# Optimization experiments

Measured on AMD Instinct MI355X. Metric: run time of the kernel, lower is better.

## Reference

```python
import jax, jax.numpy as jnp
import numpy as np

DIM = 384
PATCH = [(4, 4), (8, 8), (16, 16)]  # (width, height) per channel chunk
B, H, W = 4, 192, 192


def setup_inputs() -> dict:
    key = jax.random.key(0)
    ks = jax.random.split(key, 6)
    c = DIM
    return {
        "rgb": jax.random.normal(ks[0], (B, c, H, W), jnp.float32),
        "fre": jax.random.normal(ks[1], (B, c, H, W), jnp.float32),
        # shared BatchNorm2d (eval-mode affine) applied to both rgb and fre
        "norm_gamma": jnp.ones((c,), jnp.float32),
        "norm_beta": jnp.zeros((c,), jnp.float32),
        "norm_mean": jnp.zeros((c,), jnp.float32),
        "norm_var": jnp.ones((c,), jnp.float32),
        # qv: Conv2d(c, 2c, 1); k: Conv2d(c, c, 1)
        "qv_w": jax.random.normal(ks[2], (2 * c, c), jnp.float32) * 0.02,
        "qv_b": jnp.zeros((2 * c,), jnp.float32),
        "k_w": jax.random.normal(ks[3], (c, c), jnp.float32) * 0.02,
        "k_b": jnp.zeros((c,), jnp.float32),
        # out_conv: Conv2d(c, c, 3, padding=1, bias=False) + BN + LeakyReLU(0.2)
        "oc_w": jax.random.normal(ks[4], (c, c, 3, 3), jnp.float32) * 0.02,
        "oc_gamma": jnp.ones((c,), jnp.float32),
        "oc_beta": jnp.zeros((c,), jnp.float32),
        "oc_mean": jnp.zeros((c,), jnp.float32),
        "oc_var": jnp.ones((c,), jnp.float32),
    }


def _bn(x, g, b, m, v, eps=1e-5):
    scale = g * jax.lax.rsqrt(v + eps)
    return x * scale[None, :, None, None] + (b - m * scale)[None, :, None, None]


def _conv1x1(x, w, b):
    return jnp.einsum('bchw,oc->bohw', x, w) + b[None, :, None, None]


def _win_attn(q, k, v, ww, wh, scale):
    # q,k,v: [b, d, h, w]; window of size (wh x ww)
    b, d, h, w = q.shape
    gh, gw = h // wh, w // ww

    def to_win(t):  # -> [b, gh*gw, wh*ww, d]
        t = t.reshape(b, d, gh, wh, gw, ww).transpose(0, 2, 4, 3, 5, 1)
        return t.reshape(b, gh * gw, wh * ww, d)

    qw, kw, vw = to_win(q), to_win(k), to_win(v)
    attn = jax.nn.softmax((qw * scale) @ kw.swapaxes(-2, -1), axis=-1)
    o = (attn @ vw).reshape(b, gh, gw, wh, ww, d)
    return o.transpose(0, 5, 1, 3, 2, 4).reshape(b, d, h, w)


def reference(rgb, fre, norm_gamma, norm_beta, norm_mean, norm_var,
              qv_w, qv_b, k_w, k_b, oc_w, oc_gamma, oc_beta, oc_mean, oc_var):
    b, c, h, w = rgb.shape
    n = len(PATCH)
    d_k = c // n
    scale = d_k ** (-0.5)

    qv = _conv1x1(_bn(rgb, norm_gamma, norm_beta, norm_mean, norm_var), qv_w, qv_b)
    q, v = qv[:, :c], qv[:, c:]  # reshape(b,2,c,h,w) ordering -> first c = q, next c = v
    k = _conv1x1(_bn(fre, norm_gamma, norm_beta, norm_mean, norm_var), k_w, k_b)

    outs = []
    for i, (ww, wh) in enumerate(PATCH):
        sl = slice(i * d_k, (i + 1) * d_k)
        o = _win_attn(q[:, sl], k[:, sl], v[:, sl], ww, wh, scale) + rgb[:, sl]
        outs.append(o)
    x = jnp.concatenate(outs, axis=1)

    x = jax.lax.conv_general_dilated(x, oc_w, (1, 1), 'SAME',
                                     dimension_numbers=('NCHW', 'OIHW', 'NCHW'))
    x = _bn(x, oc_gamma, oc_beta, oc_mean, oc_var)
    return jnp.where(x >= 0, x, 0.2 * x)  # LeakyReLU(0.2)
```

## Files before the change

### kernel.cpp

```cpp
#include <hip/hip_runtime.h>
#include <stdint.h>

typedef __attribute__((ext_vector_type(8))) short short8;
typedef __attribute__((ext_vector_type(8))) unsigned short ushort8;
typedef __attribute__((ext_vector_type(4))) float f32x4;

#define MFMA(a,b,c) __builtin_amdgcn_mfma_f32_16x16x32_bf16((a),(b),(c),0,0,0)

__device__ __forceinline__ unsigned short f2bf(float f) {
  union { float f; unsigned u; } v; v.f = f;
  unsigned r = v.u + 0x7fffu + ((v.u >> 16) & 1u);
  return (unsigned short)(r >> 16);
}
__device__ __forceinline__ float bf2f(unsigned short s) {
  union { unsigned u; float f; } v; v.u = ((unsigned)s) << 16;
  return v.f;
}

__device__ __forceinline__ void g2l16(const unsigned short* g, unsigned short* l) {
  __builtin_amdgcn_global_load_lds(
      (const __attribute__((address_space(1))) unsigned int*)(g),
      (__attribute__((address_space(3))) unsigned int*)(l), 16, 0, 0);
}

__device__ __forceinline__ int vswz(int c, int key) {
  return key ^ ((((c >> 3) ^ c) & 7) << 3);
}

__global__ void nhwc_kernel(const float* __restrict__ src, unsigned short* __restrict__ dst) {
  __shared__ unsigned short T[64][72];
  int p0 = blockIdx.x * 64, c0 = blockIdx.y * 64, bb = blockIdx.z;
  const float* S = src + (size_t)bb * 384 * 36864;
  unsigned short* D = dst + (size_t)bb * 36864 * 384;
  int t = threadIdx.x;
  int pl = (t & 15) * 4;
  int r0 = t >> 4;
#pragma unroll
  for (int k = 0; k < 4; ++k) {
    int c = r0 + 16 * k;
    float4 v = *(const float4*)&S[(size_t)(c0 + c) * 36864 + p0 + pl];
    T[pl + 0][c] = f2bf(v.x); T[pl + 1][c] = f2bf(v.y);
    T[pl + 2][c] = f2bf(v.z); T[pl + 3][c] = f2bf(v.w);
  }
  __syncthreads();
  int row = t >> 2, ch = (t & 3) * 16;
  ushort8 a = *(const ushort8*)&T[row][ch];
  ushort8 b = *(const ushort8*)&T[row][ch + 8];
  uint4* d = (uint4*)&D[(size_t)(p0 + row) * 384 + c0 + ch];
  d[0] = *(uint4*)&a; d[1] = *(uint4*)&b;
}

__global__ void fold_qvk_kernel(const float* __restrict__ qv_w, const float* __restrict__ qv_b,
                                const float* __restrict__ k_w, const float* __restrict__ k_b,
                                const float* __restrict__ g, const float* __restrict__ be,
                                const float* __restrict__ mu, const float* __restrict__ var,
                                unsigned short* __restrict__ Wq, float* __restrict__ bq,
                                unsigned short* __restrict__ Wk, float* __restrict__ bk) {
  int o = blockIdx.x;
  int t = threadIdx.x;
  bool isq = o < 768;
  int oo = isq ? o : o - 768;
  const float* wrow = isq ? qv_w + (size_t)oo * 384 : k_w + (size_t)oo * 384;
  float mul = (isq && oo < 384) ? 0.08838834764831845f : 1.0f;
  float acc = 0.f;
  for (int c = t; c < 384; c += 128) {
    float sc = g[c] * rsqrtf(var[c] + 1e-5f);
    float sh = be[c] - mu[c] * sc;
    float w = wrow[c];
    acc += w * sh;
    unsigned short wb = f2bf(w * sc * mul);
    if (isq) Wq[(size_t)oo * 384 + c] = wb; else Wk[(size_t)oo * 384 + c] = wb;
  }
#pragma unroll
  for (int m = 1; m < 64; m <<= 1) acc += __shfl_xor(acc, m);
  __shared__ float part[2];
  if ((t & 63) == 0) part[t >> 6] = acc;
  __syncthreads();
  if (t == 0) {
    float b0 = isq ? qv_b[oo] : k_b[oo];
    float bias = (b0 + part[0] + part[1]) * mul;
    if (isq) bq[oo] = bias; else bk[oo] = bias;
  }
}

__global__ void fold_oc_kernel(const float* __restrict__ oc_w,
                               const float* __restrict__ g, const float* __restrict__ be,
                               const float* __restrict__ mu, const float* __restrict__ var,
                               unsigned short* __restrict__ Wc, float* __restrict__ s_oc,
                               float* __restrict__ t_oc) {
  int idx = blockIdx.x * 256 + threadIdx.x;
  if (idx < 384) {
    float sc = g[idx] * rsqrtf(var[idx] + 1e-5f);
    s_oc[idx] = sc;
    t_oc[idx] = be[idx] - mu[idx] * sc;
  }
  if (idx < 384 * 3456) {
    int o = idx / 3456, r = idx % 3456;
    int kq = r / 384, c = r % 384;
    Wc[idx] = f2bf(oc_w[((size_t)o * 384 + c) * 9 + kq]);
  }
}

__launch_bounds__(512)
__global__ void gemm1n_kernel(const unsigned short* __restrict__ XN, const unsigned short* __restrict__ W,
                              const float* __restrict__ bias, unsigned short* __restrict__ Out,
                              int OW, int OT) {
  int nwg = gridDim.x;
  int bid = blockIdx.x;
  int bi = (bid & 7) * (nwg >> 3) + (bid >> 3);
  int ot = bi % OT;
  int pt = (bi / OT) % 144;
  int bb = bi / (OT * 144);
  int obase = ot * 128, pbase = pt * 256;
  __shared__ unsigned short Ws2[2][128 * 32];
  __shared__ unsigned short Xs2[2][256 * 32];
  int tid = threadIdx.x;
  int wv = tid >> 6, lane = tid & 63;
  int l15 = lane & 15, lg = lane >> 4;
  int wc = wv & 1, wr = wv >> 1;
  f32x4 acc[4][4];
#pragma unroll
  for (int i = 0; i < 4; ++i)
#pragma unroll
    for (int j = 0; j < 4; ++j) acc[i][j] = 0.f;
  int rl = lane >> 2;
  int csw = (((lane & 3) ^ ((lane >> 3) & 3)) << 3);
  const unsigned short* Ap = W + (size_t)(obase + 16 * wv + rl) * 384 + csw;
  const unsigned short* XbN = XN + (size_t)bb * 36864 * 384;
  const unsigned short* Bp0 = XbN + (size_t)(pbase + 32 * wv + rl) * 384 + csw;
  const unsigned short* Bp1 = Bp0 + (size_t)16 * 384;
  int colsw = ((lg ^ ((l15 >> 1) & 3)) << 3);
  unsigned short* WsW = &Ws2[0][(16 * wv) * 32];
  unsigned short* XsW0 = &Xs2[0][(32 * wv) * 32];
  unsigned short* XsW1 = &Xs2[0][(32 * wv + 16) * 32];
  const int WBUF = 128 * 32, XBUF = 256 * 32;
  g2l16(Ap, WsW); g2l16(Bp0, XsW0); g2l16(Bp1, XsW1);
  Ap += 32; Bp0 += 32; Bp1 += 32;
  for (int t = 0; t < 12; ++t) {
    int cur = t & 1, nxt = cur ^ 1;
    if (t < 11) {
      g2l16(Ap, WsW + nxt * WBUF);
      g2l16(Bp0, XsW0 + nxt * XBUF);
      g2l16(Bp1, XsW1 + nxt * XBUF);
      Ap += 32; Bp0 += 32; Bp1 += 32;
      asm volatile("s_waitcnt vmcnt(3)" ::: "memory");
    } else {
      asm volatile("s_waitcnt vmcnt(0)" ::: "memory");
    }
    __builtin_amdgcn_s_barrier();
    __builtin_amdgcn_sched_barrier(0);
    const unsigned short* Wt = &Ws2[cur][0];
    const unsigned short* Xt = &Xs2[cur][0];
    short8 af[4], bf[4];
#pragma unroll
    for (int f = 0; f < 4; ++f) af[f] = *(const short8*)&Xt[(wr * 64 + f * 16 + l15) * 32 + colsw];
#pragma unroll
    for (int f = 0; f < 4; ++f) bf[f] = *(const short8*)&Wt[(wc * 64 + f * 16 + l15) * 32 + colsw];
#pragma unroll
    for (int fm = 0; fm < 4; ++fm)
#pragma unroll
      for (int fn = 0; fn < 4; ++fn)
        acc[fm][fn] = MFMA(af[fm], bf[fn], acc[fm][fn]);
    __builtin_amdgcn_s_barrier();
    __builtin_amdgcn_sched_barrier(0);
  }
  unsigned short* Ob = Out + (size_t)bb * 36864 * OW;
#pragma unroll
  for (int fn = 0; fn < 4; ++fn) {
    int o = obase + wc * 64 + fn * 16 + l15;
    float bsv = bias[o];
#pragma unroll
    for (int fm = 0; fm < 4; ++fm) {
#pragma unroll
      for (int r = 0; r < 4; ++r) {
        int p = pbase + wr * 64 + fm * 16 + lg * 4 + r;
        Ob[(size_t)p * OW + o] = f2bf(acc[fm][fn][r] + bsv);
      }
    }
  }
}

__launch_bounds__(256)
__global__ void gemm1_kernel(const float* __restrict__ X, const unsigned short* __restrict__ W,
                             const float* __restrict__ bias, unsigned short* __restrict__ Out,
                             int OW, int OT) {
  int bi = blockIdx.x;
  int ot = bi % OT;
  int pt = (bi / OT) % 288;
  int bb = bi / (OT * 288);
  int obase = ot * 128, pbase = pt * 128;
  __shared__ unsigned short As[128 * 40];
  __shared__ unsigned short Bs[128 * 40];
  int tid = threadIdx.x;
  int wv = tid >> 6, lane = tid & 63;
  int l15 = lane & 15, lg = lane >> 4;
  int pw = (wv >> 1) * 64, ow = (wv & 1) * 64;
  f32x4 acc[4][4];
#pragma unroll
  for (int i = 0; i < 4; ++i)
#pragma unroll
    for (int j = 0; j < 4; ++j) acc[i][j] = 0.f;
  const float* Xb = X + (size_t)bb * 384 * 36864;
  int arow = tid >> 1, ahalf = tid & 1;
  int bp = tid & 127, bcg0 = tid >> 7;
  for (int ks = 0; ks < 12; ++ks) {
    int c0 = ks * 32;
    __syncthreads();
    {
      const uint4* s4 = (const uint4*)(W + (size_t)(obase + arow) * 384 + c0 + ahalf * 16);
      uint4 a0 = s4[0], a1 = s4[1];
      uint4* d = (uint4*)&As[arow * 40 + ahalf * 16];
      d[0] = a0; d[1] = a1;
    }
    {
#pragma unroll
      for (int q = 0; q < 2; ++q) {
        int cg = bcg0 + q * 2;
        int cc = c0 + cg * 8;
        const float* src = Xb + (size_t)cc * 36864 + pbase + bp;
        ushort8 t8;
#pragma unroll
        for (int j = 0; j < 8; ++j) t8[j] = f2bf(src[(size_t)j * 36864]);
        *(ushort8*)&Bs[bp * 40 + cg * 8] = t8;
      }
    }
    __syncthreads();
    short8 af[4], bf[4];
#pragma unroll
    for (int f = 0; f < 4; ++f) af[f] = *(const short8*)&Bs[(pw + f * 16 + l15) * 40 + lg * 8];
#pragma unroll
    for (int f = 0; f < 4; ++f) bf[f] = *(const short8*)&As[(ow + f * 16 + l15) * 40 + lg * 8];
#pragma unroll
    for (int fm = 0; fm < 4; ++fm)
#pragma unroll
      for (int fn = 0; fn < 4; ++fn)
        acc[fm][fn] = MFMA(af[fm], bf[fn], acc[fm][fn]);
  }
  unsigned short* Ob = Out + (size_t)bb * 36864 * OW;
#pragma unroll
  for (int fn = 0; fn < 4; ++fn) {
    int o = obase + ow + fn * 16 + l15;
    float bsv = bias[o];
#pragma unroll
    for (int fm = 0; fm < 4; ++fm) {
#pragma unroll
      for (int r = 0; r < 4; ++r) {
        int p = pbase + pw + fm * 16 + lg * 4 + r;
        Ob[(size_t)p * OW + o] = f2bf(acc[fm][fn][r] + bsv);
      }
    }
  }
}

template <int MODE>
__launch_bounds__(256)
__global__ void attn_kernel(const unsigned short* qv, const unsigned short* kx,
                            const float* __restrict__ rgb, const unsigned short* __restrict__ rgbn,
                            unsigned short* xout, int padded) {
  constexpr int GB = MODE * 128;
  constexpr int NKV = (MODE == 2) ? 4 : 1;
  constexpr int NKF = (MODE == 0) ? 1 : 4;
  int bi = blockIdx.x;
  int bb = bi / 576;
  int r5 = bi % 576;
  int tid = threadIdx.x;
  int wv = tid >> 6, lane = tid & 63;
  int l15 = lane & 15, lg = lane >> 4;

  int h0, w0, qtb;
  if (MODE == 0) { int wy = r5 / 12; int wxb = (r5 % 12) * 4; h0 = wy * 4; w0 = wxb * 4; qtb = 0; }
  else if (MODE == 1) { int wy = r5 / 24; int wx = r5 % 24; h0 = wy * 8; w0 = wx * 8; qtb = 0; }
  else { int win = r5 >> 2; int qt = r5 & 3; int wy = win / 12; int wx = win % 12; h0 = wy * 16; w0 = wx * 16; qtb = qt * 64; }

  auto tok2p = [&](int t) -> int {
    if (MODE == 0) { int lw = t >> 4, tt = t & 15; return (h0 + (tt >> 2)) * 192 + w0 + lw * 4 + (tt & 3); }
    else if (MODE == 1) { return (h0 + (t >> 3)) * 192 + w0 + (t & 7); }
    else { return (h0 + (t >> 4)) * 192 + w0 + (t & 15); }
  };

  __shared__ unsigned short Qs[64 * 128];
  __shared__ unsigned short Ks[64 * 128];
  __shared__ unsigned short Vst[128 * 64];
  __shared__ unsigned short Ps[4 * 16 * 72];

  const unsigned short* qvB = qv + (size_t)bb * 36864 * 768;
  const unsigned short* kB = kx + (size_t)bb * 36864 * 384;

  for (int ch = tid; ch < 1024; ch += 256) {
    int tok = ch >> 4, c8 = (ch & 15) << 3;
    int p = tok2p(qtb + tok);
    uint4 v = *(const uint4*)(qvB + (size_t)p * 768 + GB + c8);
    *(uint4*)&Qs[tok * 128 + (c8 ^ ((tok & 7) << 3))] = v;
  }
  __syncthreads();
  short8 qf[4];
  {
    int qrow = wv * 16 + l15;
#pragma unroll
    for (int cs = 0; cs < 4; ++cs)
      qf[cs] = *(const short8*)&Qs[qrow * 128 + ((cs * 32 + lg * 8) ^ ((qrow & 7) << 3))];
  }

  float m[4], s[4];
#pragma unroll
  for (int r = 0; r < 4; ++r) { m[r] = -1e30f; s[r] = 0.f; }
  f32x4 oacc[8];
#pragma unroll
  for (int i = 0; i < 8; ++i) oacc[i] = 0.f;

  for (int kt = 0; kt < NKV; ++kt) {
    __syncthreads();
    for (int ch = tid; ch < 1024; ch += 256) {
      int tok = ch >> 4, c8 = (ch & 15) << 3;
      int p = tok2p(kt * 64 + tok);
      uint4 v = *(const uint4*)(kB + (size_t)p * 384 + GB + c8);
      *(uint4*)&Ks[tok * 128 + (c8 ^ ((tok & 7) << 3))] = v;
    }
    for (int ch = tid; ch < 1024; ch += 256) {
      int key = ch >> 4, c8 = (ch & 15) << 3;
      int p = tok2p(kt * 64 + key);
      ushort8 v = *(const ushort8*)(qvB + (size_t)p * 768 + 384 + GB + c8);
#pragma unroll
      for (int j = 0; j < 8; ++j)
        Vst[(c8 + j) * 64 + vswz(c8 + j, key)] = v[j];
    }
    __syncthreads();

    f32x4 sc[NKF];
#pragma unroll
    for (int kfi = 0; kfi < NKF; ++kfi) {
      int kf = (MODE == 0) ? wv : kfi;
      int krow = kf * 16 + l15;
      f32x4 a; a = 0.f;
#pragma unroll
      for (int cs = 0; cs < 4; ++cs) {
        short8 kfr = *(const short8*)&Ks[krow * 128 + ((cs * 32 + lg * 8) ^ ((krow & 7) << 3))];
        a = MFMA(qf[cs], kfr, a);
      }
      sc[kfi] = a;
    }

    unsigned short* Pw = Ps + wv * (16 * 72);
    float pr[4][NKF];
#pragma unroll
    for (int r = 0; r < 4; ++r) {
      float mx = -1e30f;
#pragma unroll
      for (int kfi = 0; kfi < NKF; ++kfi) mx = fmaxf(mx, sc[kfi][r]);
#pragma unroll
      for (int d = 1; d < 16; d <<= 1) mx = fmaxf(mx, __shfl_xor(mx, d));
      float mn = fmaxf(m[r], mx);
      float f = __expf(m[r] - mn);
      float ls = 0.f;
#pragma unroll
      for (int kfi = 0; kfi < NKF; ++kfi) { float e = __expf(sc[kfi][r] - mn); pr[r][kfi] = e; ls += e; }
#pragma unroll
      for (int d = 1; d < 16; d <<= 1) ls += __shfl_xor(ls, d);
      s[r] = s[r] * f + ls;
      m[r] = mn;
#pragma unroll
      for (int ct = 0; ct < 8; ++ct) oacc[ct][r] *= f;
    }
#pragma unroll
    for (int r = 0; r < 4; ++r) {
      int prow = lg * 4 + r;
#pragma unroll
      for (int kfi = 0; kfi < NKF; ++kfi) {
        int pcol = (MODE == 0) ? l15 : kfi * 16 + l15;
        Pw[prow * 72 + pcol] = f2bf(pr[r][kfi]);
      }
      if (MODE == 0) Pw[prow * 72 + 16 + l15] = 0;
    }
    constexpr int nks = (MODE == 0) ? 1 : 2;
#pragma unroll
    for (int ks = 0; ks < nks; ++ks) {
      short8 pf = *(const short8*)&Pw[l15 * 72 + ks * 32 + lg * 8];
#pragma unroll
      for (int ct = 0; ct < 8; ++ct) {
        int c = ct * 16 + l15;
        short8 vf;
        if (MODE == 0) {
          if (lg < 2) vf = *(const short8*)&Vst[c * 64 + vswz(c, wv * 16 + lg * 8)];
          else vf = 0;
        } else {
          vf = *(const short8*)&Vst[c * 64 + vswz(c, ks * 32 + lg * 8)];
        }
        oacc[ct] = MFMA(pf, vf, oacc[ct]);
      }
    }
  }

  const float* rgbB = rgb + (size_t)bb * 384 * 36864;
  const unsigned short* rgbNB = rgbn + (size_t)bb * 36864 * 384;
  unsigned short* xB = padded ? xout + (size_t)bb * 37636 * 384
                              : xout + (size_t)bb * 36864 * 768;
#pragma unroll
  for (int r = 0; r < 4; ++r) {
    int q64 = wv * 16 + lg * 4 + r;
    int p = tok2p(qtb + q64);
    float inv = 1.0f / s[r];
    size_t rowoff;
    if (padded) {
      int h = p / 192, w = p % 192;
      rowoff = (size_t)((h + 1) * 194 + (w + 1)) * 384;
    } else {
      rowoff = (size_t)p * 768;
    }
#pragma unroll
    for (int ct = 0; ct < 8; ++ct) {
      int c = GB + ct * 16 + l15;
      float res = padded ? bf2f(rgbNB[(size_t)p * 384 + c]) : rgbB[(size_t)c * 36864 + p];
      float val = oacc[ct][r] * inv + res;
      xB[rowoff + c] = f2bf(val);
    }
  }
}

__global__ void zero_border_kernel(unsigned short* __restrict__ xpad) {
  int bi = blockIdx.x;
  int bb = bi / 772, i = bi % 772;
  int h, w;
  if (i < 194) { h = 0; w = i; }
  else if (i < 388) { h = 193; w = i - 194; }
  else if (i < 580) { w = 0; h = i - 388 + 1; }
  else { w = 193; h = i - 580 + 1; }
  int t = threadIdx.x;
  if (t < 48) {
    uint4 z = {0, 0, 0, 0};
    uint4* row = (uint4*)(xpad + ((size_t)bb * 37636 + h * 194 + w) * 384);
    row[t] = z;
  }
}

__launch_bounds__(512)
__global__ void conv3d_kernel(const unsigned short* __restrict__ Xp,
                              const unsigned short* __restrict__ Wc,
                              const float* __restrict__ s_oc, const float* __restrict__ t_oc,
                              float* __restrict__ Out) {
  int bid = blockIdx.x;
  int bi = (bid & 7) * 216 + (bid >> 3);
  int ot = bi % 3;
  int pt = (bi / 3) % 144;
  int bb = bi / 432;
  int obase = ot * 128, pbase = pt * 256;
  __shared__ unsigned short Ws2[2][128 * 32];
  __shared__ unsigned short Xs2[2][256 * 32];
  int tid = threadIdx.x;
  int wv = tid >> 6, lane = tid & 63;
  int l15 = lane & 15, lg = lane >> 4;
  int wc = wv & 1, wr = wv >> 1;
  f32x4 acc[4][4];
#pragma unroll
  for (int i = 0; i < 4; ++i)
#pragma unroll
    for (int j = 0; j < 4; ++j) acc[i][j] = 0.f;
  int rl = lane >> 2;
  int csw = (((lane & 3) ^ ((lane >> 3) & 3)) << 3);
  const unsigned short* Ap = Wc + (size_t)(obase + 16 * wv + rl) * 3456 + csw;
  int p0 = pbase + 32 * wv + rl;
  int p1 = p0 + 16;
  const unsigned short* Xb = Xp + (size_t)bb * 37636 * 384;
  const unsigned short* Bp0 = Xb + (size_t)((p0 / 192 + 1) * 194 + (p0 % 192 + 1) - 195) * 384 + csw;
  const unsigned short* Bp1 = Xb + (size_t)((p1 / 192 + 1) * 194 + (p1 % 192 + 1) - 195) * 384 + csw;
  int colsw = ((lg ^ ((l15 >> 1) & 3)) << 3);
  unsigned short* WsW = &Ws2[0][(16 * wv) * 32];
  unsigned short* XsW0 = &Xs2[0][(32 * wv) * 32];
  unsigned short* XsW1 = &Xs2[0][(32 * wv + 16) * 32];
  const int WBUF = 128 * 32, XBUF = 256 * 32;
  g2l16(Ap, WsW); g2l16(Bp0, XsW0); g2l16(Bp1, XsW1);
  Ap += 32; Bp0 += 32; Bp1 += 32;
  for (int t = 0; t < 108; ++t) {
    int cur = t & 1, nxt = cur ^ 1;
    if (t < 107) {
      g2l16(Ap, WsW + nxt * WBUF);
      g2l16(Bp0, XsW0 + nxt * XBUF);
      g2l16(Bp1, XsW1 + nxt * XBUF);
      Ap += 32; Bp0 += 32; Bp1 += 32;
      if (t == 34 || t == 70) { Bp0 += 73344; Bp1 += 73344; }
      asm volatile("s_waitcnt vmcnt(3)" ::: "memory");
    } else {
      asm volatile("s_waitcnt vmcnt(0)" ::: "memory");
    }
    __builtin_amdgcn_s_barrier();
    __builtin_amdgcn_sched_barrier(0);
    const unsigned short* Wt = &Ws2[cur][0];
    const unsigned short* Xt = &Xs2[cur][0];
    short8 af[4], bf2[4];
#pragma unroll
    for (int f = 0; f < 4; ++f) af[f] = *(const short8*)&Wt[(wc * 64 + f * 16 + l15) * 32 + colsw];
#pragma unroll
    for (int f = 0; f < 4; ++f) bf2[f] = *(const short8*)&Xt[(wr * 64 + f * 16 + l15) * 32 + colsw];
#pragma unroll
    for (int fm = 0; fm < 4; ++fm)
#pragma unroll
      for (int fn = 0; fn < 4; ++fn)
        acc[fm][fn] = MFMA(af[fm], bf2[fn], acc[fm][fn]);
    __builtin_amdgcn_s_barrier();
    __builtin_amdgcn_sched_barrier(0);
  }
  float* Ob = Out + (size_t)bb * 384 * 36864;
#pragma unroll
  for (int fm = 0; fm < 4; ++fm) {
#pragma unroll
    for (int r = 0; r < 4; ++r) {
      int o = obase + wc * 64 + fm * 16 + lg * 4 + r;
      float sv = s_oc[o], tv = t_oc[o];
#pragma unroll
      for (int fn = 0; fn < 4; ++fn) {
        int p = pbase + wr * 64 + fn * 16 + l15;
        float y = acc[fm][fn][r] * sv + tv;
        Ob[(size_t)o * 36864 + p] = (y >= 0.f) ? y : 0.2f * y;
      }
    }
  }
}

__launch_bounds__(256)
__global__ void conv3_kernel(const unsigned short* __restrict__ X,
                             const unsigned short* __restrict__ Wc,
                             const float* __restrict__ s_oc, const float* __restrict__ t_oc,
                             float* __restrict__ Out) {
  int bi = blockIdx.x;
  int pt = bi % 288;
  int ot = (bi / 288) % 3;
  int bb = bi / 864;
  int obase = ot * 128, pbase = pt * 128;
  __shared__ unsigned short As[128 * 40];
  __shared__ unsigned short Bs[128 * 40];
  int tid = threadIdx.x;
  int wv = tid >> 6, lane = tid & 63;
  int l15 = lane & 15, lg = lane >> 4;
  int ow = (wv & 1) * 64, pw = (wv >> 1) * 64;
  f32x4 acc[4][4];
#pragma unroll
  for (int i = 0; i < 4; ++i)
#pragma unroll
    for (int j = 0; j < 4; ++j) acc[i][j] = 0.f;
  int arow = tid >> 1, ahalf = tid & 1;
  int sp = pbase + arow;
  int sh = sp / 192, sw = sp % 192;
  const unsigned short* Xb = X + (size_t)bb * 36864 * 768;
  for (int ksi = 0; ksi < 108; ++ksi) {
    int kq = ksi / 12;
    int c0 = (ksi % 12) * 32;
    int dh = kq / 3 - 1, dw = kq % 3 - 1;
    __syncthreads();
    {
      const uint4* s4 = (const uint4*)(Wc + (size_t)(obase + arow) * 3456 + kq * 384 + c0 + ahalf * 16);
      uint4 a0 = s4[0], a1 = s4[1];
      uint4* d = (uint4*)&As[arow * 40 + ahalf * 16];
      d[0] = a0; d[1] = a1;
    }
    {
      int hh = sh + dh, ww2 = sw + dw;
      uint4 b0 = {0, 0, 0, 0}, b1 = {0, 0, 0, 0};
      if ((unsigned)hh < 192u && (unsigned)ww2 < 192u) {
        const uint4* s4 = (const uint4*)(Xb + (size_t)(hh * 192 + ww2) * 768 + c0 + ahalf * 16);
        b0 = s4[0]; b1 = s4[1];
      }
      uint4* d = (uint4*)&Bs[arow * 40 + ahalf * 16];
      d[0] = b0; d[1] = b1;
    }
    __syncthreads();
    short8 af[4], bf2[4];
#pragma unroll
    for (int f = 0; f < 4; ++f) af[f] = *(const short8*)&As[(ow + f * 16 + l15) * 40 + lg * 8];
#pragma unroll
    for (int f = 0; f < 4; ++f) bf2[f] = *(const short8*)&Bs[(pw + f * 16 + l15) * 40 + lg * 8];
#pragma unroll
    for (int fm = 0; fm < 4; ++fm)
#pragma unroll
      for (int fn = 0; fn < 4; ++fn)
        acc[fm][fn] = MFMA(af[fm], bf2[fn], acc[fm][fn]);
  }
  float* Ob = Out + (size_t)bb * 384 * 36864;
#pragma unroll
  for (int fm = 0; fm < 4; ++fm) {
#pragma unroll
    for (int r = 0; r < 4; ++r) {
      int o = obase + ow + fm * 16 + lg * 4 + r;
      float sv = s_oc[o], tv = t_oc[o];
#pragma unroll
      for (int fn = 0; fn < 4; ++fn) {
        int p = pbase + pw + fn * 16 + l15;
        float y = acc[fm][fn][r] * sv + tv;
        Ob[(size_t)o * 36864 + p] = (y >= 0.f) ? y : 0.2f * y;
      }
    }
  }
}

extern "C" void kernel_launch(void* const* d_in, const int* in_sizes, int n_in,
                              void* d_out, int out_size, void* d_ws, size_t ws_size,
                              hipStream_t stream) {
  const float* rgb  = (const float*)d_in[0];
  const float* fre  = (const float*)d_in[1];
  const float* ng   = (const float*)d_in[2];
  const float* nb   = (const float*)d_in[3];
  const float* nm   = (const float*)d_in[4];
  const float* nv   = (const float*)d_in[5];
  const float* qv_w = (const float*)d_in[6];
  const float* qv_b = (const float*)d_in[7];
  const float* k_w  = (const float*)d_in[8];
  const float* k_b  = (const float*)d_in[9];
  const float* oc_w = (const float*)d_in[10];
  const float* oc_g = (const float*)d_in[11];
  const float* oc_b = (const float*)d_in[12];
  const float* oc_m = (const float*)d_in[13];
  const float* oc_v = (const float*)d_in[14];

  char* ws = (char*)d_ws;
  const size_t QV_B   = 226492416;
  const size_t K_B    = 113246208;
  const size_t XPAD_B = 115617792;
  const size_t RGBN_B = 113246208;
  size_t off = 0;
  unsigned short* qvbuf = (unsigned short*)(ws + off); off += QV_B;
  unsigned short* kbuf  = (unsigned short*)(ws + off); off += K_B;
  size_t dyn_off = off;
  unsigned short* xpad = (unsigned short*)(ws + dyn_off);
  unsigned short* rgbN = (unsigned short*)(ws + dyn_off + XPAD_B);
  const size_t WEIGHTS_B = 589824 + 294912 + 2654208 + 3072 + 1536 + 1536 + 1536;
  bool fast = (ws_size >= dyn_off + XPAD_B + RGBN_B + WEIGHTS_B);
  if (fast) off += XPAD_B + RGBN_B;
  unsigned short* Wq = (unsigned short*)(ws + off); off += 589824;
  unsigned short* Wk = (unsigned short*)(ws + off); off += 294912;
  unsigned short* Wc = (unsigned short*)(ws + off); off += 2654208;
  float* bq  = (float*)(ws + off); off += 3072;
  float* bk  = (float*)(ws + off); off += 1536;
  float* soc = (float*)(ws + off); off += 1536;
  float* toc = (float*)(ws + off); off += 1536;
  float* out = (float*)d_out;

  fold_qvk_kernel<<<dim3(1152), dim3(128), 0, stream>>>(qv_w, qv_b, k_w, k_b, ng, nb, nm, nv, Wq, bq, Wk, bk);
  fold_oc_kernel<<<dim3(5184), dim3(256), 0, stream>>>(oc_w, oc_g, oc_b, oc_m, oc_v, Wc, soc, toc);

  if (fast) {
    unsigned short* freN = xpad;
    nhwc_kernel<<<dim3(576, 6, 4), dim3(256), 0, stream>>>(rgb, rgbN);
    nhwc_kernel<<<dim3(576, 6, 4), dim3(256), 0, stream>>>(fre, freN);
    gemm1n_kernel<<<dim3(3456), dim3(512), 0, stream>>>(rgbN, Wq, bq, qvbuf, 768, 6);
    gemm1n_kernel<<<dim3(1728), dim3(512), 0, stream>>>(freN, Wk, bk, kbuf, 384, 3);
    zero_border_kernel<<<dim3(4 * 772), dim3(64), 0, stream>>>(xpad);
    attn_kernel<0><<<dim3(2304), dim3(256), 0, stream>>>(qvbuf, kbuf, rgb, rgbN, xpad, 1);
    attn_kernel<1><<<dim3(2304), dim3(256), 0, stream>>>(qvbuf, kbuf, rgb, rgbN, xpad, 1);
    attn_kernel<2><<<dim3(2304), dim3(256), 0, stream>>>(qvbuf, kbuf, rgb, rgbN, xpad, 1);
    conv3d_kernel<<<dim3(1728), dim3(512), 0, stream>>>(xpad, Wc, soc, toc, out);
  } else {
    gemm1_kernel<<<dim3(4 * 288 * 6), dim3(256), 0, stream>>>(rgb, Wq, bq, qvbuf, 768, 6);
    gemm1_kernel<<<dim3(4 * 288 * 3), dim3(256), 0, stream>>>(fre, Wk, bk, kbuf, 384, 3);
    attn_kernel<0><<<dim3(2304), dim3(256), 0, stream>>>(qvbuf, kbuf, rgb, qvbuf, qvbuf, 0);
    attn_kernel<1><<<dim3(2304), dim3(256), 0, stream>>>(qvbuf, kbuf, rgb, qvbuf, qvbuf, 0);
    attn_kernel<2><<<dim3(2304), dim3(256), 0, stream>>>(qvbuf, kbuf, rgb, qvbuf, qvbuf, 0);
    conv3_kernel<<<dim3(4 * 3 * 288), dim3(256), 0, stream>>>(qvbuf, Wc, soc, toc, out);
  }
}
```

Before: 1.219 ms.

## Restructure 3x3 conv GEMM main loop into interleaved half-tile phases with priority

The implicit-GEMM conv kernel now stages two 32-wide K slices per iteration (54 iterations instead of 108) into split LDS half-buffers. Each iteration runs four MFMA phases, and the global-to-LDS copies and LDS fragment reads for the next phase are issued between them. s_setprio and barriers bracket the MFMA blocks so memory traffic overlaps with matrix math, ping-pong style. This doubles LDS use and adds barriers per iteration. The base pointer arithmetic is simplified equivalently.

New measurement: 1.345 ms. 10.4% more time.

```diff
diff --git a/kernel.cpp b/kernel.cpp
--- a/kernel.cpp
+++ b/kernel.cpp
@@ -433,7 +433,7 @@
 }
 
 __launch_bounds__(512)
-__global__ void conv3d_kernel(const unsigned short* __restrict__ Xp,
+__global__ void conv3e_kernel(const unsigned short* __restrict__ Xp,
                               const unsigned short* __restrict__ Wc,
                               const float* __restrict__ s_oc, const float* __restrict__ t_oc,
                               float* __restrict__ Out) {
@@ -443,8 +443,8 @@
   int pt = (bi / 3) % 144;
   int bb = bi / 432;
   int obase = ot * 128, pbase = pt * 256;
-  __shared__ unsigned short Ws2[2][128 * 32];
-  __shared__ unsigned short Xs2[2][256 * 32];
+  __shared__ unsigned short Ah[2][2][128 * 32];
+  __shared__ unsigned short Bh[2][2][256 * 32];
   int tid = threadIdx.x;
   int wv = tid >> 6, lane = tid & 63;
   int l15 = lane & 15, lg = lane >> 4;
@@ -460,44 +460,95 @@
   int p0 = pbase + 32 * wv + rl;
   int p1 = p0 + 16;
   const unsigned short* Xb = Xp + (size_t)bb * 37636 * 384;
-  const unsigned short* Bp0 = Xb + (size_t)((p0 / 192 + 1) * 194 + (p0 % 192 + 1) - 195) * 384 + csw;
-  const unsigned short* Bp1 = Xb + (size_t)((p1 / 192 + 1) * 194 + (p1 % 192 + 1) - 195) * 384 + csw;
+  const unsigned short* Bp0 = Xb + (size_t)((p0 / 192) * 194 + (p0 % 192)) * 384 + csw;
+  const unsigned short* Bp1 = Xb + (size_t)((p1 / 192) * 194 + (p1 % 192)) * 384 + csw;
   int colsw = ((lg ^ ((l15 >> 1) & 3)) << 3);
-  unsigned short* WsW = &Ws2[0][(16 * wv) * 32];
-  unsigned short* XsW0 = &Xs2[0][(32 * wv) * 32];
-  unsigned short* XsW1 = &Xs2[0][(32 * wv + 16) * 32];
-  const int WBUF = 128 * 32, XBUF = 256 * 32;
-  g2l16(Ap, WsW); g2l16(Bp0, XsW0); g2l16(Bp1, XsW1);
-  Ap += 32; Bp0 += 32; Bp1 += 32;
-  for (int t = 0; t < 108; ++t) {
+  unsigned short* AsW = &Ah[0][0][(16 * wv) * 32];
+  unsigned short* BsW0 = &Bh[0][0][(32 * wv) * 32];
+  unsigned short* BsW1 = &Bh[0][0][(32 * wv + 16) * 32];
+  const int AHS = 128 * 32, BHS = 256 * 32;
+
+  auto STAGE = [&](int slot, int half) {
+    g2l16(Ap, AsW + (slot * 2 + half) * AHS);
+    g2l16(Bp0, BsW0 + (slot * 2 + half) * BHS);
+    g2l16(Bp1, BsW1 + (slot * 2 + half) * BHS);
+    Ap += 32; Bp0 += 32; Bp1 += 32;
+  };
+
+  STAGE(0, 0); STAGE(0, 1);
+  asm volatile("s_waitcnt vmcnt(3)" ::: "memory");
+  __builtin_amdgcn_s_barrier();
+
+  int aoff = (wc * 64 + l15) * 32 + colsw;
+  int boff = (wr * 64 + l15) * 32 + colsw;
+
+#define PH_IN()  __builtin_amdgcn_s_barrier();                              \
+                 asm volatile("s_waitcnt lgkmcnt(0)" ::: "memory");         \
+                 __builtin_amdgcn_sched_barrier(0);                         \
+                 __builtin_amdgcn_s_setprio(1);
+#define PH_OUT() __builtin_amdgcn_s_setprio(0);                             \
+                 __builtin_amdgcn_sched_barrier(0);                         \
+                 __builtin_amdgcn_s_barrier();
+
+  for (int t = 0; t < 54; ++t) {
     int cur = t & 1, nxt = cur ^ 1;
-    if (t < 107) {
-      g2l16(Ap, WsW + nxt * WBUF);
-      g2l16(Bp0, XsW0 + nxt * XBUF);
-      g2l16(Bp1, XsW1 + nxt * XBUF);
-      Ap += 32; Bp0 += 32; Bp1 += 32;
-      if (t == 34 || t == 70) { Bp0 += 73344; Bp1 += 73344; }
-      asm volatile("s_waitcnt vmcnt(3)" ::: "memory");
-    } else {
-      asm volatile("s_waitcnt vmcnt(0)" ::: "memory");
-    }
-    __builtin_amdgcn_s_barrier();
-    __builtin_amdgcn_sched_barrier(0);
-    const unsigned short* Wt = &Ws2[cur][0];
-    const unsigned short* Xt = &Xs2[cur][0];
-    short8 af[4], bf2[4];
-#pragma unroll
-    for (int f = 0; f < 4; ++f) af[f] = *(const short8*)&Wt[(wc * 64 + f * 16 + l15) * 32 + colsw];
-#pragma unroll
-    for (int f = 0; f < 4; ++f) bf2[f] = *(const short8*)&Xt[(wr * 64 + f * 16 + l15) * 32 + colsw];
-#pragma unroll
-    for (int fm = 0; fm < 4; ++fm)
-#pragma unroll
-      for (int fn = 0; fn < 4; ++fn)
-        acc[fm][fn] = MFMA(af[fm], bf2[fn], acc[fm][fn]);
-    __builtin_amdgcn_s_barrier();
-    __builtin_amdgcn_sched_barrier(0);
-  }
+    const unsigned short* A0 = &Ah[cur][0][0];
+    const unsigned short* A1 = &Ah[cur][1][0];
+    const unsigned short* B0 = &Bh[cur][0][0];
+    const unsigned short* B1 = &Bh[cur][1][0];
+    short8 a0, a1, b0, b1, b2, b3;
+    b0 = *(const short8*)&B0[boff + 0 * 512];
+    b1 = *(const short8*)&B0[boff + 1 * 512];
+    b2 = *(const short8*)&B0[boff + 2 * 512];
+    b3 = *(const short8*)&B0[boff + 3 * 512];
+    a0 = *(const short8*)&A0[aoff + 0 * 512];
+    a1 = *(const short8*)&A0[aoff + 1 * 512];
+    if (t < 53) STAGE(nxt, 0);
+    PH_IN();
+    acc[0][0] = MFMA(a0, b0, acc[0][0]); acc[0][1] = MFMA(a0, b1, acc[0][1]);
+    acc[0][2] = MFMA(a0, b2, acc[0][2]); acc[0][3] = MFMA(a0, b3, acc[0][3]);
+    acc[1][0] = MFMA(a1, b0, acc[1][0]); acc[1][1] = MFMA(a1, b1, acc[1][1]);
+    acc[1][2] = MFMA(a1, b2, acc[1][2]); acc[1][3] = MFMA(a1, b3, acc[1][3]);
+    PH_OUT();
+    a0 = *(const short8*)&A0[aoff + 2 * 512];
+    a1 = *(const short8*)&A0[aoff + 3 * 512];
+    if (t < 53) asm volatile("s_waitcnt vmcnt(3)" ::: "memory");
+    else        asm volatile("s_waitcnt vmcnt(0)" ::: "memory");
+    PH_IN();
+    acc[2][0] = MFMA(a0, b0, acc[2][0]); acc[2][1] = MFMA(a0, b1, acc[2][1]);
+    acc[2][2] = MFMA(a0, b2, acc[2][2]); acc[2][3] = MFMA(a0, b3, acc[2][3]);
+    acc[3][0] = MFMA(a1, b0, acc[3][0]); acc[3][1] = MFMA(a1, b1, acc[3][1]);
+    acc[3][2] = MFMA(a1, b2, acc[3][2]); acc[3][3] = MFMA(a1, b3, acc[3][3]);
+    PH_OUT();
+    b0 = *(const short8*)&B1[boff + 0 * 512];
+    b1 = *(const short8*)&B1[boff + 1 * 512];
+    b2 = *(const short8*)&B1[boff + 2 * 512];
+    b3 = *(const short8*)&B1[boff + 3 * 512];
+    a0 = *(const short8*)&A1[aoff + 0 * 512];
+    a1 = *(const short8*)&A1[aoff + 1 * 512];
+    if (t < 53) {
+      STAGE(nxt, 1);
+      if (t == 16 || t == 34) { Bp0 += 73344; Bp1 += 73344; }
+    }
+    PH_IN();
+    acc[0][0] = MFMA(a0, b0, acc[0][0]); acc[0][1] = MFMA(a0, b1, acc[0][1]);
+    acc[0][2] = MFMA(a0, b2, acc[0][2]); acc[0][3] = MFMA(a0, b3, acc[0][3]);
+    acc[1][0] = MFMA(a1, b0, acc[1][0]); acc[1][1] = MFMA(a1, b1, acc[1][1]);
+    acc[1][2] = MFMA(a1, b2, acc[1][2]); acc[1][3] = MFMA(a1, b3, acc[1][3]);
+    PH_OUT();
+    a0 = *(const short8*)&A1[aoff + 2 * 512];
+    a1 = *(const short8*)&A1[aoff + 3 * 512];
+    if (t < 53) asm volatile("s_waitcnt vmcnt(3)" ::: "memory");
+    PH_IN();
+    acc[2][0] = MFMA(a0, b0, acc[2][0]); acc[2][1] = MFMA(a0, b1, acc[2][1]);
+    acc[2][2] = MFMA(a0, b2, acc[2][2]); acc[2][3] = MFMA(a0, b3, acc[2][3]);
+    acc[3][0] = MFMA(a1, b0, acc[3][0]); acc[3][1] = MFMA(a1, b1, acc[3][1]);
+    acc[3][2] = MFMA(a1, b2, acc[3][2]); acc[3][3] = MFMA(a1, b3, acc[3][3]);
+    PH_OUT();
+  }
+#undef PH_IN
+#undef PH_OUT
+
   float* Ob = Out + (size_t)bb * 384 * 36864;
 #pragma unroll
   for (int fm = 0; fm < 4; ++fm) {
@@ -645,7 +696,7 @@
     attn_kernel<0><<<dim3(2304), dim3(256), 0, stream>>>(qvbuf, kbuf, rgb, rgbN, xpad, 1);
     attn_kernel<1><<<dim3(2304), dim3(256), 0, stream>>>(qvbuf, kbuf, rgb, rgbN, xpad, 1);
     attn_kernel<2><<<dim3(2304), dim3(256), 0, stream>>>(qvbuf, kbuf, rgb, rgbN, xpad, 1);
-    conv3d_kernel<<<dim3(1728), dim3(512), 0, stream>>>(xpad, Wc, soc, toc, out);
+    conv3e_kernel<<<dim3(1728), dim3(512), 0, stream>>>(xpad, Wc, soc, toc, out);
   } else {
     gemm1_kernel<<<dim3(4 * 288 * 6), dim3(256), 0, stream>>>(rgb, Wq, bq, qvbuf, 768, 6);
     gemm1_kernel<<<dim3(4 * 288 * 3), dim3(256), 0, stream>>>(fre, Wk, bk, kbuf, 384, 3);
```
